# Kernel optimization log

Measured on AMD Instinct MI355X. Metric: run time of the kernel, lower is better.

Reference implementation:

```python
import jax, jax.numpy as jnp
import numpy as np

B, I, H = 16384, 512, 512


def setup_inputs() -> dict:
    key = jax.random.key(0)
    ks = jax.random.split(key, 16)
    s_w = 1.0 / np.sqrt(I)  # torch Linear default init scale (uniform bound)
    s_u = 1.0 / np.sqrt(H)
    d = {
        "u": jax.random.normal(ks[0], (B, I), jnp.float32),
        "h": jax.random.normal(ks[1], (B, H), jnp.float32),
        "c": jax.random.normal(ks[2], (B, H), jnp.float32),
        "Wi": jax.random.normal(ks[3], (H, I), jnp.float32) * s_w,
        "bWi": jax.random.normal(ks[4], (H,), jnp.float32) * s_w,
        "Wf": jax.random.normal(ks[5], (H, I), jnp.float32) * s_w,
        "bWf": jax.random.normal(ks[6], (H,), jnp.float32) * s_w,
        "Wg": jax.random.normal(ks[7], (H, I), jnp.float32) * s_w,
        "bWg": jax.random.normal(ks[8], (H,), jnp.float32) * s_w,
        "Wo": jax.random.normal(ks[9], (H, I), jnp.float32) * s_w,
        "bWo": jax.random.normal(ks[10], (H,), jnp.float32) * s_w,
        "Ui": jax.random.normal(ks[11], (H, H), jnp.float32) * s_u,
        "Uf": jax.random.normal(ks[12], (H, H), jnp.float32) * s_u,
        "Ug": jax.random.normal(ks[13], (H, H), jnp.float32) * s_u,
        "Uo": jax.random.normal(ks[14], (H, H), jnp.float32) * s_u,
        "bi": jnp.zeros((H,), jnp.float32),
        "bf": jnp.zeros((H,), jnp.float32),
        "bg": jnp.zeros((H,), jnp.float32),
        "bo": jnp.zeros((H,), jnp.float32),
    }
    return d


def reference(u, h, c, Wi, bWi, Wf, bWf, Wg, bWg, Wo, bWo,
              Ui, Uf, Ug, Uo, bi, bf, bg, bo):
    # Fuse 4 input projections and 4 hidden projections into two GEMMs
    # each producing [B, 4H]; math identical to 8 separate Linears.
    W = jnp.concatenate([Wi, Wf, Wg, Wo], axis=0)        # [4H, I]
    U = jnp.concatenate([Ui, Uf, Ug, Uo], axis=0)        # [4H, H]
    bW = jnp.concatenate([bWi, bWf, bWg, bWo], axis=0)   # Linear biases
    bE = jnp.concatenate([bi, bf, bg, bo], axis=0)       # extra b_* params
    z = u @ W.T + h @ U.T + bW + bE                      # [B, 4H]
    zi, zf, zg, zo = jnp.split(z, 4, axis=-1)
    i = jax.nn.sigmoid(zi)
    f = jax.nn.sigmoid(zf)
    g = jnp.tanh(zg)
    o = jax.nn.sigmoid(zo)
    c_next = f * c + i * g
    h_next = o * jnp.tanh(c_next)
    return (h_next, c_next)
```

## Files before the change

kernel.cpp:

```cpp
#include <hip/hip_runtime.h>
#include <hip/hip_bf16.h>
#include <cstddef>
#include <cstdint>


#define BDIM 16384
#define HDIM 512

typedef __attribute__((ext_vector_type(8))) short bf16x8;
typedef __attribute__((ext_vector_type(4))) float f32x4;

struct Params {
  const float* u;
  const float* h;
  const float* c;
  const float* W[4];
  const float* U[4];
  const float* bW[4];
  const float* bE[4];
  float* outh;
  float* outc;
};

__device__ __forceinline__ float sigmoidf_(float x) {
  return 1.0f / (1.0f + __expf(-x));
}
__device__ __forceinline__ float tanhf_(float x) {
  return 2.0f / (1.0f + __expf(-2.0f * x)) - 1.0f;
}

__device__ __forceinline__ void async16(const void* g, void* l) {
  __builtin_amdgcn_global_load_lds((const __attribute__((address_space(1))) void*)g,
                                   (__attribute__((address_space(3))) void*)l,
                                   16, 0, 0);
}

__device__ __forceinline__ bf16x8 cvt8(f32x4 a, f32x4 b) {
  bf16x8 r;
#pragma unroll
  for (int j = 0; j < 4; ++j) {
    __hip_bfloat16 t = __float2bfloat16(a[j]);
    r[j] = *reinterpret_cast<short*>(&t);
  }
#pragma unroll
  for (int j = 0; j < 4; ++j) {
    __hip_bfloat16 t = __float2bfloat16(b[j]);
    r[4 + j] = *reinterpret_cast<short*>(&t);
  }
  return r;
}

__global__ void cvt_x_kernel(const float* __restrict__ u, const float* __restrict__ h,
                             __hip_bfloat16* __restrict__ Xbf) {
  const size_t e = ((size_t)blockIdx.x * 512 + threadIdx.x) * 8;
  const int r = (int)(e >> 10);
  const int cidx = (int)(e & 1023);
  const float* s = (cidx < 512) ? (u + (size_t)r * 512 + cidx)
                                : (h + (size_t)r * 512 + (cidx - 512));
  f32x4 v0 = *(const f32x4*)s;
  f32x4 v1 = *(const f32x4*)(s + 4);
  *(bf16x8*)(Xbf + e) = cvt8(v0, v1);
}

__global__ void cvt_w_kernel(Params p, __hip_bfloat16* __restrict__ Wbf,
                             float* __restrict__ biasC) {
  const size_t gt = (size_t)blockIdx.x * 512 + threadIdx.x;
  const size_t e = gt * 8;
  const int g = (int)(e >> 19);
  const int rem = (int)(e & 524287);
  const int hcol = rem >> 10;
  const int k = rem & 1023;
  const float* s = (k < 512) ? (p.W[g] + (size_t)hcol * 512 + k)
                             : (p.U[g] + (size_t)hcol * 512 + (k - 512));
  f32x4 v0 = *(const f32x4*)s;
  f32x4 v1 = *(const f32x4*)(s + 4);
  *(bf16x8*)(Wbf + e) = cvt8(v0, v1);
  if (gt < 2048) {
    const int bg = (int)(gt >> 9), hh = (int)(gt & 511);
    biasC[gt] = p.bW[bg][hh] + p.bE[bg][hh];
  }
}

__launch_bounds__(512, 2)
__global__ void lstm_main_kernel(const __hip_bfloat16* __restrict__ Xbf,
                                 const __hip_bfloat16* __restrict__ Wbf,
                                 const float* __restrict__ biasC,
                                 const float* __restrict__ c,
                                 float* __restrict__ outh,
                                 float* __restrict__ outc) {
  __shared__ char smem[131072];

  const int tid = threadIdx.x;
  const int w   = tid >> 6;
  const int l   = tid & 63;
  const int wm  = w >> 2;
  const int wh  = w & 3;

  const int swz = (blockIdx.x & 7) * 64 + (blockIdx.x >> 3);
  const int m_tile = swz & 63;
  const int h_tile = swz >> 6;
  const int rowA0 = m_tile * 256;
  const int nrow0 = h_tile * 64;

  const int rsub = l >> 3;
  const int slot = (l & 7) ^ rsub;
  const int gW = w >> 1;
  const int hrel0 = (w & 1) * 32;

  f32x4 acc[4][8] = {};

  auto stage = [&](int kt, char* bufA, char* bufW) {
    const int kc = kt * 64;
#pragma unroll
    for (int j = 0; j < 4; ++j) {
      const int rit = w * 32 + j * 8 + rsub;
      const __hip_bfloat16* gp = Xbf + (size_t)(rowA0 + rit) * 1024 + kc + slot * 8;
      async16(gp, bufA + (w * 32 + j * 8) * 128);
    }
#pragma unroll
    for (int j = 0; j < 4; ++j) {
      const int hr = hrel0 + j * 8 + rsub;
      const __hip_bfloat16* gp =
          Wbf + (size_t)(gW * 512 + nrow0 + hr) * 1024 + kc + slot * 8;
      async16(gp, bufW + (w * 32 + j * 8) * 128);
    }
  };

  const int xr = (l & 7) << 4;

  auto compute = [&](const char* bufA, const char* bufW) {
#pragma unroll
    for (int kk = 0; kk < 2; ++kk) {
      const int kb = (kk * 64 + (l >> 4) * 16) ^ xr;
      bf16x8 a[8];
#pragma unroll
      for (int mf = 0; mf < 8; ++mf)
        a[mf] = *(const bf16x8*)(bufA + (wm * 128 + mf * 16 + (l & 15)) * 128 + kb);
#pragma unroll
      for (int g = 0; g < 4; ++g) {
        bf16x8 b = *(const bf16x8*)(bufW + (g * 64 + wh * 16 + (l & 15)) * 128 + kb);
#pragma unroll
        for (int mf = 0; mf < 8; ++mf)
          acc[g][mf] = __builtin_amdgcn_mfma_f32_16x16x32_bf16(a[mf], b, acc[g][mf], 0, 0, 0);
      }
    }
  };

  stage(0, smem, smem + 32768);
  __syncthreads();
  int cur = 0;
  for (int kt = 0; kt < 16; ++kt) {
    char* bA = smem + cur * 65536;
    char* nA = smem + (cur ^ 1) * 65536;
    if (kt < 15) stage(kt + 1, nA, nA + 32768);
    compute(bA, bA + 32768);
    __syncthreads();
    cur ^= 1;
  }

  const int lr = (l >> 4) * 4;
  const int lc = l & 15;
  const int hc = nrow0 + wh * 16 + lc;
  const float bzi = biasC[0 * 512 + hc];
  const float bzf = biasC[1 * 512 + hc];
  const float bzg = biasC[2 * 512 + hc];
  const float bzo = biasC[3 * 512 + hc];
#pragma unroll
  for (int mf = 0; mf < 8; ++mf) {
#pragma unroll
    for (int j = 0; j < 4; ++j) {
      const int row = rowA0 + wm * 128 + mf * 16 + lr + j;
      const float zi = acc[0][mf][j] + bzi;
      const float zf = acc[1][mf][j] + bzf;
      const float zg = acc[2][mf][j] + bzg;
      const float zo = acc[3][mf][j] + bzo;
      const float ig = sigmoidf_(zi);
      const float fg = sigmoidf_(zf);
      const float gg = tanhf_(zg);
      const float og = sigmoidf_(zo);
      const size_t idx = (size_t)row * 512 + hc;
      const float cv = c[idx];
      const float cn = fg * cv + ig * gg;
      const float hn = og * tanhf_(cn);
      outh[idx] = hn;
      outc[idx] = cn;
    }
  }
}

__launch_bounds__(256, 2)
__global__ void lstm_legacy_kernel(Params p) {
  __shared__ char smem[32768];
  __shared__ float biasLDS[4][32];

  const int tid = threadIdx.x;
  const int w   = tid >> 6;
  const int l   = tid & 63;
  const int m_tile = blockIdx.x & 127;
  const int h_tile = blockIdx.x >> 7;

  char* smemA = smem;
  char* smemW = smem + 16384;
  const int rowA0 = m_tile * 128;
  const int nrow0 = h_tile * 32;

  if (tid < 128) {
    const int g = tid >> 5, hh = tid & 31;
    const int hc = nrow0 + hh;
    biasLDS[g][hh] = p.bW[g][hc] + p.bE[g][hc];
  }

  const int sr = tid >> 3;
  const int sc = tid & 7;
  const int wcol = (sc * 16) ^ ((sr & 7) << 4);

  f32x4 acc[4][2][2] = {};
  f32x4 rg[16];

  auto load_tile = [&](int kt) {
    const float* sA = (kt < 8) ? p.u : p.h;
    const int kc = (kt & 7) * 64;
#pragma unroll
    for (int cc = 0; cc < 4; ++cc) {
      const float* gp = sA + (size_t)(rowA0 + cc * 32 + sr) * 512 + kc + sc * 8;
      rg[cc * 2]     = *(const f32x4*)gp;
      rg[cc * 2 + 1] = *(const f32x4*)(gp + 4);
    }
#pragma unroll
    for (int cc = 0; cc < 4; ++cc) {
      const float* sW = (kt < 8) ? p.W[cc] : p.U[cc];
      const float* gp = sW + (size_t)(nrow0 + sr) * 512 + kc + sc * 8;
      rg[8 + cc * 2]     = *(const f32x4*)gp;
      rg[8 + cc * 2 + 1] = *(const f32x4*)(gp + 4);
    }
  };

  auto write_tile = [&]() {
#pragma unroll
    for (int cc = 0; cc < 4; ++cc)
      *(bf16x8*)(smemA + (cc * 32 + sr) * 128 + wcol) = cvt8(rg[cc * 2], rg[cc * 2 + 1]);
#pragma unroll
    for (int cc = 0; cc < 4; ++cc)
      *(bf16x8*)(smemW + (cc * 32 + sr) * 128 + wcol) = cvt8(rg[8 + cc * 2], rg[8 + cc * 2 + 1]);
  };

  const int xr = (l & 7) << 4;

  auto compute = [&]() {
#pragma unroll
    for (int kk = 0; kk < 2; ++kk) {
      const int kb = (kk * 64 + (l >> 4) * 16) ^ xr;
      bf16x8 a0 = *(const bf16x8*)(smemA + (w * 32 +      (l & 15)) * 128 + kb);
      bf16x8 a1 = *(const bf16x8*)(smemA + (w * 32 + 16 + (l & 15)) * 128 + kb);
#pragma unroll
      for (int g = 0; g < 4; ++g) {
#pragma unroll
        for (int ni = 0; ni < 2; ++ni) {
          bf16x8 b = *(const bf16x8*)(smemW + (g * 32 + ni * 16 + (l & 15)) * 128 + kb);
          acc[g][0][ni] = __builtin_amdgcn_mfma_f32_16x16x32_bf16(a0, b, acc[g][0][ni], 0, 0, 0);
          acc[g][1][ni] = __builtin_amdgcn_mfma_f32_16x16x32_bf16(a1, b, acc[g][1][ni], 0, 0, 0);
        }
      }
    }
  };

  load_tile(0);
  for (int kt = 0; kt < 16; ++kt) {
    write_tile();
    __syncthreads();
    if (kt < 15) load_tile(kt + 1);
    compute();
    __syncthreads();
  }

  const int lr = (l >> 4) * 4;
  const int lc = l & 15;
#pragma unroll
  for (int mi = 0; mi < 2; ++mi) {
#pragma unroll
    for (int j = 0; j < 4; ++j) {
      const int row = rowA0 + w * 32 + mi * 16 + lr + j;
#pragma unroll
      for (int ni = 0; ni < 2; ++ni) {
        const int hc = nrow0 + ni * 16 + lc;
        const int bcol = ni * 16 + lc;
        const float zi = acc[0][mi][ni][j] + biasLDS[0][bcol];
        const float zf = acc[1][mi][ni][j] + biasLDS[1][bcol];
        const float zg = acc[2][mi][ni][j] + biasLDS[2][bcol];
        const float zo = acc[3][mi][ni][j] + biasLDS[3][bcol];
        const float ig = sigmoidf_(zi);
        const float fg = sigmoidf_(zf);
        const float gg = tanhf_(zg);
        const float og = sigmoidf_(zo);
        const size_t idx = (size_t)row * 512 + hc;
        const float cv = p.c[idx];
        const float cn = fg * cv + ig * gg;
        const float hn = og * tanhf_(cn);
        p.outh[idx] = hn;
        p.outc[idx] = cn;
      }
    }
  }
}

extern "C" void kernel_launch(void* const* d_in, const int* in_sizes, int n_in,
                              void* d_out, int out_size, void* d_ws, size_t ws_size,
                              hipStream_t stream) {
  Params p;
  p.u = (const float*)d_in[0];
  p.h = (const float*)d_in[1];
  p.c = (const float*)d_in[2];
  p.W[0] = (const float*)d_in[3];
  p.bW[0] = (const float*)d_in[4];
  p.W[1] = (const float*)d_in[5];
  p.bW[1] = (const float*)d_in[6];
  p.W[2] = (const float*)d_in[7];
  p.bW[2] = (const float*)d_in[8];
  p.W[3] = (const float*)d_in[9];
  p.bW[3] = (const float*)d_in[10];
  p.U[0] = (const float*)d_in[11];
  p.U[1] = (const float*)d_in[12];
  p.U[2] = (const float*)d_in[13];
  p.U[3] = (const float*)d_in[14];
  p.bE[0] = (const float*)d_in[15];
  p.bE[1] = (const float*)d_in[16];
  p.bE[2] = (const float*)d_in[17];
  p.bE[3] = (const float*)d_in[18];
  p.outh = (float*)d_out;
  p.outc = (float*)d_out + (size_t)BDIM * HDIM;

  const size_t X_BYTES = (size_t)BDIM * 1024 * 2;
  const size_t W_BYTES = (size_t)4 * 512 * 1024 * 2;
  const size_t B_BYTES = 2048 * 4;
  if (ws_size >= X_BYTES + W_BYTES + B_BYTES) {
    __hip_bfloat16* Xbf = (__hip_bfloat16*)d_ws;
    __hip_bfloat16* Wbf = (__hip_bfloat16*)((char*)d_ws + X_BYTES);
    float* biasC = (float*)((char*)d_ws + X_BYTES + W_BYTES);

    hipLaunchKernelGGL(cvt_x_kernel, dim3(4096), dim3(512), 0, stream, p.u, p.h, Xbf);
    hipLaunchKernelGGL(cvt_w_kernel, dim3(512), dim3(512), 0, stream, p, Wbf, biasC);
    hipLaunchKernelGGL(lstm_main_kernel, dim3(512), dim3(512), 0, stream,
                       Xbf, Wbf, biasC, p.c, p.outh, p.outc);
  } else {
    hipLaunchKernelGGL(lstm_legacy_kernel, dim3(2048), dim3(256), 0, stream, p);
  }
}
```

Before: 98.95 us.

## Restructure GEMM main loop into phased ping-pong schedule with setprio and barriers

The K loop is split into four phases per tile. Each phase loads half the A fragments (and the B fragments once per k-step), interleaves the async global-to-LDS prefetch of the next tile across phases, and issues MFMAs at raised wave priority with explicit s_barrier, sched_barrier and waitcnt. Global pointers are precomputed outside the loop. The aim is to overlap LDS reads, global prefetch and MFMA issue across waves, and to cut register pressure from holding eight A fragments. The cost is many more barriers per tile, which can stall waves if the phases are unbalanced.

After: 104.1 us. 1.05x slower.

```diff
diff --git a/kernel.cpp b/kernel.cpp
--- a/kernel.cpp
+++ b/kernel.cpp
@@ -107,56 +107,79 @@
   const int gW = w >> 1;
   const int hrel0 = (w & 1) * 32;
 
+  const __hip_bfloat16* gpA[4];
+  const __hip_bfloat16* gpW[4];
+#pragma unroll
+  for (int j = 0; j < 4; ++j) {
+    gpA[j] = Xbf + (size_t)(rowA0 + w * 32 + j * 8 + rsub) * 1024 + slot * 8;
+    gpW[j] = Wbf + (size_t)(gW * 512 + nrow0 + hrel0 + j * 8 + rsub) * 1024 + slot * 8;
+  }
+
   f32x4 acc[4][8] = {};
 
-  auto stage = [&](int kt, char* bufA, char* bufW) {
-    const int kc = kt * 64;
-#pragma unroll
-    for (int j = 0; j < 4; ++j) {
-      const int rit = w * 32 + j * 8 + rsub;
-      const __hip_bfloat16* gp = Xbf + (size_t)(rowA0 + rit) * 1024 + kc + slot * 8;
-      async16(gp, bufA + (w * 32 + j * 8) * 128);
-    }
-#pragma unroll
-    for (int j = 0; j < 4; ++j) {
-      const int hr = hrel0 + j * 8 + rsub;
-      const __hip_bfloat16* gp =
-          Wbf + (size_t)(gW * 512 + nrow0 + hr) * 1024 + kc + slot * 8;
-      async16(gp, bufW + (w * 32 + j * 8) * 128);
-    }
-  };
-
-  const int xr = (l & 7) << 4;
-
-  auto compute = [&](const char* bufA, const char* bufW) {
-#pragma unroll
-    for (int kk = 0; kk < 2; ++kk) {
-      const int kb = (kk * 64 + (l >> 4) * 16) ^ xr;
-      bf16x8 a[8];
-#pragma unroll
-      for (int mf = 0; mf < 8; ++mf)
-        a[mf] = *(const bf16x8*)(bufA + (wm * 128 + mf * 16 + (l & 15)) * 128 + kb);
-#pragma unroll
-      for (int g = 0; g < 4; ++g) {
-        bf16x8 b = *(const bf16x8*)(bufW + (g * 64 + wh * 16 + (l & 15)) * 128 + kb);
-#pragma unroll
-        for (int mf = 0; mf < 8; ++mf)
-          acc[g][mf] = __builtin_amdgcn_mfma_f32_16x16x32_bf16(a[mf], b, acc[g][mf], 0, 0, 0);
+  const int xr  = (l & 7) << 4;
+  const int ar  = l & 15;
+  const int kbase = (l >> 4) * 16;
+
+#define STAGE_A(T)                                                        \
+  {                                                                       \
+    char* db = smem + (((T) & 1) << 16);                                  \
+    _Pragma("unroll") for (int j = 0; j < 4; ++j)                         \
+        async16(gpA[j] + (T) * 64, db + (w * 32 + j * 8) * 128);          \
+  }
+#define STAGE_W(T)                                                        \
+  {                                                                       \
+    char* db = smem + (((T) & 1) << 16) + 32768;                          \
+    _Pragma("unroll") for (int j = 0; j < 4; ++j)                         \
+        async16(gpW[j] + (T) * 64, db + (w * 32 + j * 8) * 128);          \
+  }
+
+  STAGE_A(0)
+  STAGE_W(0)
+  asm volatile("s_waitcnt vmcnt(0)" ::: "memory");
+  __builtin_amdgcn_sched_barrier(0);
+  __builtin_amdgcn_s_barrier();
+
+  for (int t = 0; t < 16; ++t) {
+    const char* bufA = smem + ((t & 1) << 16);
+    const char* bufW = bufA + 32768;
+    bf16x8 bw[4];
+    bf16x8 av[4];
+#pragma unroll
+    for (int ph = 0; ph < 4; ++ph) {
+      const int kk = ph >> 1;
+      const int mh = ph & 1;
+      const int kb = (kk * 64 + kbase) ^ xr;
+#pragma unroll
+      for (int i = 0; i < 4; ++i)
+        av[i] = *(const bf16x8*)(bufA + (wm * 128 + (mh * 4 + i) * 16 + ar) * 128 + kb);
+      if (mh == 0) {
+#pragma unroll
+        for (int g = 0; g < 4; ++g)
+          bw[g] = *(const bf16x8*)(bufW + (g * 64 + wh * 16 + ar) * 128 + kb);
       }
-    }
-  };
-
-  stage(0, smem, smem + 32768);
-  __syncthreads();
-  int cur = 0;
-  for (int kt = 0; kt < 16; ++kt) {
-    char* bA = smem + cur * 65536;
-    char* nA = smem + (cur ^ 1) * 65536;
-    if (kt < 15) stage(kt + 1, nA, nA + 32768);
-    compute(bA, bA + 32768);
-    __syncthreads();
-    cur ^= 1;
-  }
+      if (ph == 0 && t < 15) STAGE_A(t + 1)
+      if (ph == 1 && t < 15) STAGE_W(t + 1)
+      asm volatile("" ::: "memory");
+      __builtin_amdgcn_s_barrier();
+      asm volatile("s_waitcnt lgkmcnt(0)" ::: "memory");
+      __builtin_amdgcn_sched_barrier(0);
+      __builtin_amdgcn_s_setprio(1);
+#pragma unroll
+      for (int g = 0; g < 4; ++g)
+#pragma unroll
+        for (int i = 0; i < 4; ++i)
+          acc[g][mh * 4 + i] = __builtin_amdgcn_mfma_f32_16x16x32_bf16(
+              av[i], bw[g], acc[g][mh * 4 + i], 0, 0, 0);
+      __builtin_amdgcn_s_setprio(0);
+      __builtin_amdgcn_sched_barrier(0);
+    }
+    asm volatile("s_waitcnt vmcnt(0)" ::: "memory");
+    __builtin_amdgcn_sched_barrier(0);
+    __builtin_amdgcn_s_barrier();
+  }
+#undef STAGE_A
+#undef STAGE_W
 
   const int lr = (l >> 4) * 4;
   const int lc = l & 15;
```

## Load weight fragments directly from global into registers, halve LDS footprint

Applied to the files above, without the earlier changes.

The B (weight) operand is no longer staged through shared memory. Each lane now reads its MFMA fragment straight from global memory into registers, with a register double-buffer (wa/wb) that prefetches the next k-half. Only the activation tile is still double-buffered in LDS, so LDS use drops from 128KB to 64KB. This aims to cut LDS traffic and raise possible occupancy, at the cost of uncoalesced-ish direct global loads whose latency must be hidden behind the MFMAs.

New measurement: 124.4 us. +25.8%, slower.

```diff
diff --git a/kernel.cpp b/kernel.cpp
--- a/kernel.cpp
+++ b/kernel.cpp
@@ -88,7 +88,7 @@
                                  const float* __restrict__ c,
                                  float* __restrict__ outh,
                                  float* __restrict__ outc) {
-  __shared__ char smem[131072];
+  __shared__ char smem[65536];
 
   const int tid = threadIdx.x;
   const int w   = tid >> 6;
@@ -104,59 +104,75 @@
 
   const int rsub = l >> 3;
   const int slot = (l & 7) ^ rsub;
-  const int gW = w >> 1;
-  const int hrel0 = (w & 1) * 32;
+
+  const __hip_bfloat16* gpA[4];
+#pragma unroll
+  for (int j = 0; j < 4; ++j)
+    gpA[j] = Xbf + (size_t)(rowA0 + w * 32 + j * 8 + rsub) * 1024 + slot * 8;
+
+  const __hip_bfloat16* wp[4];
+#pragma unroll
+  for (int g = 0; g < 4; ++g)
+    wp[g] = Wbf + (size_t)(g * 512 + nrow0 + wh * 16 + (l & 15)) * 1024 + (l >> 4) * 8;
 
   f32x4 acc[4][8] = {};
 
-  auto stage = [&](int kt, char* bufA, char* bufW) {
-    const int kc = kt * 64;
-#pragma unroll
-    for (int j = 0; j < 4; ++j) {
-      const int rit = w * 32 + j * 8 + rsub;
-      const __hip_bfloat16* gp = Xbf + (size_t)(rowA0 + rit) * 1024 + kc + slot * 8;
-      async16(gp, bufA + (w * 32 + j * 8) * 128);
-    }
-#pragma unroll
-    for (int j = 0; j < 4; ++j) {
-      const int hr = hrel0 + j * 8 + rsub;
-      const __hip_bfloat16* gp =
-          Wbf + (size_t)(gW * 512 + nrow0 + hr) * 1024 + kc + slot * 8;
-      async16(gp, bufW + (w * 32 + j * 8) * 128);
-    }
-  };
-
   const int xr = (l & 7) << 4;
-
-  auto compute = [&](const char* bufA, const char* bufW) {
-#pragma unroll
-    for (int kk = 0; kk < 2; ++kk) {
-      const int kb = (kk * 64 + (l >> 4) * 16) ^ xr;
-      bf16x8 a[8];
+  const int ar = l & 15;
+  const int kbase = (l >> 4) * 16;
+
+#define STAGE_A(T)                                                        \
+  {                                                                       \
+    char* db = smem + (((T) & 1) << 15);                                  \
+    _Pragma("unroll") for (int j = 0; j < 4; ++j)                         \
+        async16(gpA[j] + (T) * 64, db + (w * 32 + j * 8) * 128);          \
+  }
+
+  bf16x8 wa[4], wb[4];
+#pragma unroll
+  for (int g = 0; g < 4; ++g) wa[g] = *(const bf16x8*)(wp[g]);
+  STAGE_A(0)
+  __syncthreads();
+
+  for (int t = 0; t < 16; ++t) {
+    const char* bufA = smem + ((t & 1) << 15);
+    if (t < 15) STAGE_A(t + 1)
+
+#pragma unroll
+    for (int g = 0; g < 4; ++g)
+      wb[g] = *(const bf16x8*)(wp[g] + t * 64 + 32);
+    {
+      const int kb = kbase ^ xr;
+      bf16x8 av[8];
 #pragma unroll
       for (int mf = 0; mf < 8; ++mf)
-        a[mf] = *(const bf16x8*)(bufA + (wm * 128 + mf * 16 + (l & 15)) * 128 + kb);
-#pragma unroll
-      for (int g = 0; g < 4; ++g) {
-        bf16x8 b = *(const bf16x8*)(bufW + (g * 64 + wh * 16 + (l & 15)) * 128 + kb);
+        av[mf] = *(const bf16x8*)(bufA + (wm * 128 + mf * 16 + ar) * 128 + kb);
+#pragma unroll
+      for (int g = 0; g < 4; ++g)
 #pragma unroll
         for (int mf = 0; mf < 8; ++mf)
-          acc[g][mf] = __builtin_amdgcn_mfma_f32_16x16x32_bf16(a[mf], b, acc[g][mf], 0, 0, 0);
-      }
-    }
-  };
-
-  stage(0, smem, smem + 32768);
-  __syncthreads();
-  int cur = 0;
-  for (int kt = 0; kt < 16; ++kt) {
-    char* bA = smem + cur * 65536;
-    char* nA = smem + (cur ^ 1) * 65536;
-    if (kt < 15) stage(kt + 1, nA, nA + 32768);
-    compute(bA, bA + 32768);
+          acc[g][mf] = __builtin_amdgcn_mfma_f32_16x16x32_bf16(av[mf], wa[g], acc[g][mf], 0, 0, 0);
+    }
+    if (t < 15) {
+#pragma unroll
+      for (int g = 0; g < 4; ++g)
+        wa[g] = *(const bf16x8*)(wp[g] + (t + 1) * 64);
+    }
+    {
+      const int kb = (64 + kbase) ^ xr;
+      bf16x8 av[8];
+#pragma unroll
+      for (int mf = 0; mf < 8; ++mf)
+        av[mf] = *(const bf16x8*)(bufA + (wm * 128 + mf * 16 + ar) * 128 + kb);
+#pragma unroll
+      for (int g = 0; g < 4; ++g)
+#pragma unroll
+        for (int mf = 0; mf < 8; ++mf)
+          acc[g][mf] = __builtin_amdgcn_mfma_f32_16x16x32_bf16(av[mf], wb[g], acc[g][mf], 0, 0, 0);
+    }
     __syncthreads();
-    cur ^= 1;
-  }
+  }
+#undef STAGE_A
 
   const int lr = (l >> 4) * 4;
   const int lc = l & 15;
```

## Interleave async global-to-LDS loads with quarter-tile MFMA phases using manual waitcnts

Applied to the files above, without the earlier changes.

Replaces the simple per-k-tile stage/compute/syncthreads loop with a hand-scheduled pipeline. Each k-tile is split into four MFMA quadrants (A half × gate half), and the next tile's async loads are issued in pieces between them, with explicit vmcnt/lgkmcnt waits, raw s_barrier and sched_barrier fences. s_setprio is raised around the MFMA blocks. The aim is to overlap global loads and LDS reads with matrix math and to avoid full-drain syncs, at the cost of fragile hand-counted waitcnts and higher register pressure from holding separate bLo/bHi fragments.

Result: no change. 99.31 us (+0.4%).

```diff
diff --git a/kernel.cpp b/kernel.cpp
--- a/kernel.cpp
+++ b/kernel.cpp
@@ -81,6 +81,34 @@
   }
 }
 
+#define VM4 asm volatile("s_waitcnt vmcnt(4)" ::: "memory")
+#define VM2 asm volatile("s_waitcnt vmcnt(2)" ::: "memory")
+#define VM0 asm volatile("s_waitcnt vmcnt(0)" ::: "memory")
+#define LG0 asm volatile("s_waitcnt lgkmcnt(0)" ::: "memory")
+#define BARRIER do { __builtin_amdgcn_s_barrier(); asm volatile("" ::: "memory"); } while (0)
+#define FENCE __builtin_amdgcn_sched_barrier(0)
+
+#define READ_A(BUF, MH, DST)                                                         \
+  _Pragma("unroll") for (int mf = 0; mf < 4; ++mf) {                                 \
+    DST[mf * 2 + 0] = *(const bf16x8*)((BUF) + (wm * 128 + (MH) * 64 + mf * 16 + ar) * 128 + kb0); \
+    DST[mf * 2 + 1] = *(const bf16x8*)((BUF) + (wm * 128 + (MH) * 64 + mf * 16 + ar) * 128 + kb1); \
+  }
+#define READ_W(BUF, GH, DST)                                                         \
+  _Pragma("unroll") for (int g2 = 0; g2 < 2; ++g2) {                                 \
+    DST[g2 * 2 + 0] = *(const bf16x8*)((BUF) + (((GH) * 2 + g2) * 64 + wh * 16 + ar) * 128 + kb0); \
+    DST[g2 * 2 + 1] = *(const bf16x8*)((BUF) + (((GH) * 2 + g2) * 64 + wh * 16 + ar) * 128 + kb1); \
+  }
+#define MMAC(MH, GH, AF, BF)                                                         \
+  do {                                                                               \
+    __builtin_amdgcn_s_setprio(1);                                                   \
+    _Pragma("unroll") for (int g2 = 0; g2 < 2; ++g2)                                 \
+    _Pragma("unroll") for (int mf = 0; mf < 4; ++mf)                                 \
+    _Pragma("unroll") for (int kk = 0; kk < 2; ++kk)                                 \
+      acc[(GH) * 2 + g2][(MH) * 4 + mf] = __builtin_amdgcn_mfma_f32_16x16x32_bf16(   \
+          AF[mf * 2 + kk], BF[g2 * 2 + kk], acc[(GH) * 2 + g2][(MH) * 4 + mf], 0, 0, 0); \
+    __builtin_amdgcn_s_setprio(0);                                                   \
+  } while (0)
+
 __launch_bounds__(512, 2)
 __global__ void lstm_main_kernel(const __hip_bfloat16* __restrict__ Xbf,
                                  const __hip_bfloat16* __restrict__ Wbf,
@@ -104,58 +132,86 @@
 
   const int rsub = l >> 3;
   const int slot = (l & 7) ^ rsub;
-  const int gW = w >> 1;
-  const int hrel0 = (w & 1) * 32;
+  const int wofs = w * 8 * 128;
+
+  const __hip_bfloat16* pA = Xbf + (size_t)(rowA0 + w * 8 + rsub) * 1024 + slot * 8;
+  const __hip_bfloat16* pW = Wbf + (size_t)(nrow0 + w * 8 + rsub) * 1024 + slot * 8;
 
   f32x4 acc[4][8] = {};
 
-  auto stage = [&](int kt, char* bufA, char* bufW) {
-    const int kc = kt * 64;
-#pragma unroll
-    for (int j = 0; j < 4; ++j) {
-      const int rit = w * 32 + j * 8 + rsub;
-      const __hip_bfloat16* gp = Xbf + (size_t)(rowA0 + rit) * 1024 + kc + slot * 8;
-      async16(gp, bufA + (w * 32 + j * 8) * 128);
-    }
-#pragma unroll
-    for (int j = 0; j < 4; ++j) {
-      const int hr = hrel0 + j * 8 + rsub;
-      const __hip_bfloat16* gp =
-          Wbf + (size_t)(gW * 512 + nrow0 + hr) * 1024 + kc + slot * 8;
-      async16(gp, bufW + (w * 32 + j * 8) * 128);
-    }
+  const int xr  = (l & 7) << 4;
+  const int ar  = l & 15;
+  const int kb0 = (((l >> 4) * 16)) ^ xr;
+  const int kb1 = (64 + ((l >> 4) * 16)) ^ xr;
+
+  auto stA = [&](const __hip_bfloat16* base, char* sl, int mh, int r) {
+    async16(base + (size_t)(mh * 128 + r * 64) * 1024,
+            sl + (mh * 128 + r * 64) * 128 + wofs);
   };
-
-  const int xr = (l & 7) << 4;
-
-  auto compute = [&](const char* bufA, const char* bufW) {
-#pragma unroll
-    for (int kk = 0; kk < 2; ++kk) {
-      const int kb = (kk * 64 + (l >> 4) * 16) ^ xr;
-      bf16x8 a[8];
-#pragma unroll
-      for (int mf = 0; mf < 8; ++mf)
-        a[mf] = *(const bf16x8*)(bufA + (wm * 128 + mf * 16 + (l & 15)) * 128 + kb);
-#pragma unroll
-      for (int g = 0; g < 4; ++g) {
-        bf16x8 b = *(const bf16x8*)(bufW + (g * 64 + wh * 16 + (l & 15)) * 128 + kb);
-#pragma unroll
-        for (int mf = 0; mf < 8; ++mf)
-          acc[g][mf] = __builtin_amdgcn_mfma_f32_16x16x32_bf16(a[mf], b, acc[g][mf], 0, 0, 0);
-      }
-    }
+  auto stW = [&](const __hip_bfloat16* base, char* sl, int g) {
+    async16(base + (size_t)(g * 512) * 1024,
+            sl + 32768 + g * 64 * 128 + wofs);
   };
 
-  stage(0, smem, smem + 32768);
-  __syncthreads();
-  int cur = 0;
-  for (int kt = 0; kt < 16; ++kt) {
-    char* bA = smem + cur * 65536;
-    char* nA = smem + (cur ^ 1) * 65536;
-    if (kt < 15) stage(kt + 1, nA, nA + 32768);
-    compute(bA, bA + 32768);
-    __syncthreads();
-    cur ^= 1;
+  {
+    char* s0 = smem;
+    stA(pA, s0, 0, 0); stA(pA, s0, 1, 0);
+    stW(pW, s0, 0);    stW(pW, s0, 1);
+    stW(pW, s0, 2);    stW(pW, s0, 3);
+    stA(pA, s0, 0, 1); stA(pA, s0, 1, 1);
+  }
+
+  bf16x8 aF[8], bLo[4], bHi[4];
+  const __hip_bfloat16* npA = pA + 64;
+  const __hip_bfloat16* npW = pW + 64;
+
+  for (int t = 0; t < 15; ++t) {
+    const char* bufA = smem + ((t & 1) << 16);
+    const char* bufW = bufA + 32768;
+    char* ns = smem + (((t + 1) & 1) << 16);
+
+    VM4; BARRIER;
+    READ_A(bufA, 0, aF);
+    READ_W(bufW, 0, bLo);
+    stA(npA, ns, 0, 0); stA(npA, ns, 1, 0);
+    LG0; FENCE;
+    MMAC(0, 0, aF, bLo); FENCE;
+
+    VM4; BARRIER;
+    READ_W(bufW, 1, bHi);
+    stW(npW, ns, 0); stW(npW, ns, 1);
+    LG0; FENCE;
+    MMAC(0, 1, aF, bHi); FENCE;
+
+    VM4; BARRIER;
+    READ_A(bufA, 1, aF);
+    stW(npW, ns, 2); stW(npW, ns, 3);
+    LG0; FENCE;
+    MMAC(1, 0, aF, bLo); FENCE;
+
+    stA(npA, ns, 0, 1); stA(npA, ns, 1, 1);
+    MMAC(1, 1, aF, bHi); FENCE;
+
+    npA += 64; npW += 64;
+  }
+
+  {
+    const char* bufA = smem + (1 << 16);
+    const char* bufW = bufA + 32768;
+    VM4; BARRIER;
+    READ_A(bufA, 0, aF);
+    READ_W(bufW, 0, bLo);
+    LG0; FENCE;
+    MMAC(0, 0, aF, bLo); FENCE;
+    VM2; BARRIER;
+    READ_W(bufW, 1, bHi);
+    LG0; FENCE;
+    MMAC(0, 1, aF, bHi); FENCE;
+    VM0; BARRIER;
+    READ_A(bufA, 1, aF);
+    LG0; FENCE;
+    MMAC(1, 0, aF, bLo); FENCE;
+    MMAC(1, 1, aF, bHi);
   }
 
   const int lr = (l >> 4) * 4;
@@ -206,8 +262,8 @@
 
   if (tid < 128) {
     const int g = tid >> 5, hh = tid & 31;
-    const int hc = nrow0 + hh;
-    biasLDS[g][hh] = p.bW[g][hc] + p.bE[g][hc];
+    const int hcb = nrow0 + hh;
+    biasLDS[g][hh] = p.bW[g][hcb] + p.bE[g][hcb];
   }
 
   const int sr = tid >> 3;
@@ -282,7 +338,7 @@
       const int row = rowA0 + w * 32 + mi * 16 + lr + j;
 #pragma unroll
       for (int ni = 0; ni < 2; ++ni) {
-        const int hc = nrow0 + ni * 16 + lc;
+        const int hcc = nrow0 + ni * 16 + lc;
         const int bcol = ni * 16 + lc;
         const float zi = acc[0][mi][ni][j] + biasLDS[0][bcol];
         const float zf = acc[1][mi][ni][j] + biasLDS[1][bcol];
@@ -292,7 +348,7 @@
         const float fg = sigmoidf_(zf);
         const float gg = tanhf_(zg);
         const float og = sigmoidf_(zo);
-        const size_t idx = (size_t)row * 512 + hc;
+        const size_t idx = (size_t)row * 512 + hcc;
         const float cv = p.c[idx];
         const float cn = fg * cv + ig * gg;
         const float hn = og * tanhf_(cn);
```
